# Optimization experiments

Hardware: AMD Instinct MI355X
Metric: run time of the kernel (lower is better)

Reference implementation:

```python
import jax, jax.numpy as jnp
import numpy as np

N = 50000      # nodes
E = 800000     # edges (avg degree 16)
IN = 128       # input feature dim
H = 128        # hidden dim (all layers output H; out_channels unused in source)
DROP_P = 0.5


def setup_inputs() -> dict:
    key = jax.random.key(0)
    ks = jax.random.split(key, 8)
    s_in = 1.0 / np.sqrt(IN).astype(np.float32)
    s_h = 1.0 / np.sqrt(H).astype(np.float32)
    return {
        "x": jax.random.normal(ks[0], (N, IN), jnp.float32),
        "edge_index": jax.random.randint(ks[1], (2, E), 0, N, dtype=jnp.int32),
        "Wl0": jax.random.normal(ks[2], (H, IN), jnp.float32) * s_in,
        "bl0": jnp.zeros((H,), jnp.float32),
        "Wr0": jax.random.normal(ks[3], (H, IN), jnp.float32) * s_in,
        "Wl1": jax.random.normal(ks[4], (H, H), jnp.float32) * s_h,
        "bl1": jnp.zeros((H,), jnp.float32),
        "Wr1": jax.random.normal(ks[5], (H, H), jnp.float32) * s_h,
    }


def _sage_conv(x, src, dst, Wl, bl, Wr):
    # mean-aggregate neighbor messages: gather x[src], scatter-add to dst
    agg = jax.ops.segment_sum(x[src], dst, num_segments=N)          # [N, D]
    deg = jax.ops.segment_sum(jnp.ones((src.shape[0],), x.dtype), dst,
                              num_segments=N)                        # [N]
    agg = agg / jnp.maximum(deg, 1.0)[:, None]                       # scatter_mean (0 for isolated nodes)
    # PyG SAGEConv: lin_l(agg) (with bias) + lin_r(x) (no bias)
    return agg @ Wl.T + bl + x @ Wr.T


def reference(x, edge_index, Wl0, bl0, Wr0, Wl1, bl1, Wr1):
    src, dst = edge_index[0], edge_index[1]
    h = _sage_conv(x, src, dst, Wl0, bl0, Wr0)
    h = jax.nn.relu(h)
    # dropout(p=0.5, training=True) with a fixed key for determinism
    keep = jax.random.bernoulli(jax.random.key(42), 1.0 - DROP_P, h.shape)
    h = jnp.where(keep, h / (1.0 - DROP_P), 0.0)
    out = _sage_conv(h, src, dst, Wl1, bl1, Wr1)
    return out
```

## Files before the change

kernel.cpp:

```cpp
#include <hip/hip_runtime.h>
#include <hip/hip_bf16.h>


#define HDIM 128
#define KDIM 256
#define NBUK 256
#define BNODE 196
#define BCH 2048

typedef __attribute__((ext_vector_type(8))) short bshort8;
typedef __attribute__((ext_vector_type(4))) float f32x4;

__device__ __forceinline__ ushort f2b(float f) {
  __hip_bfloat16 h = __float2bfloat16(f);
  return *(ushort*)&h;
}
__device__ __forceinline__ float blo(unsigned int v) { return __uint_as_float(v << 16); }
__device__ __forceinline__ float bhi(unsigned int v) { return __uint_as_float(v & 0xffff0000u); }
__device__ __forceinline__ unsigned int pack2(float lo, float hi) {
  return (unsigned int)f2b(lo) | ((unsigned int)f2b(hi) << 16);
}

__device__ __forceinline__ unsigned int tf_rotl(unsigned int x, int d) {
  return (x << d) | (x >> (32 - d));
}
__device__ __forceinline__ bool dropout_keep(unsigned int j) {
  unsigned int x0 = 0u, x1 = j;
  const unsigned int ks0 = 0u, ks1 = 42u, ks2 = 0x1BD11BDAu ^ 0u ^ 42u;
  x0 += ks0; x1 += ks1;
#define TF_R(r) { x0 += x1; x1 = tf_rotl(x1, (r)); x1 ^= x0; }
  TF_R(13) TF_R(15) TF_R(26) TF_R(6)
  x0 += ks1; x1 += ks2 + 1u;
  TF_R(17) TF_R(29) TF_R(16) TF_R(24)
  x0 += ks2; x1 += ks0 + 2u;
  TF_R(13) TF_R(15) TF_R(26) TF_R(6)
  x0 += ks0; x1 += ks1 + 3u;
  TF_R(17) TF_R(29) TF_R(16) TF_R(24)
  x0 += ks1; x1 += ks2 + 4u;
  TF_R(13) TF_R(15) TF_R(26) TF_R(6)
  x0 += ks2; x1 += ks0 + 5u;
#undef TF_R
  unsigned int r = x0 ^ x1;
  float u = __uint_as_float((r >> 9) | 0x3f800000u) - 1.0f;
  return u < 0.5f;
}

__global__ __launch_bounds__(256) void bhist_k(const int* __restrict__ dst,
                                               int* __restrict__ bucketCount, int E) {
  __shared__ int h[NBUK];
  h[threadIdx.x] = 0;
  __syncthreads();
  int begin = blockIdx.x * BCH;
  int n = min(BCH, E - begin);
  for (int i = threadIdx.x; i < n; i += 256) atomicAdd(&h[dst[begin + i] / BNODE], 1);
  __syncthreads();
  if (h[threadIdx.x]) atomicAdd(&bucketCount[threadIdx.x], h[threadIdx.x]);
}

__global__ __launch_bounds__(256) void bscan_k(const int* __restrict__ bucketCount,
                                               int* __restrict__ bucketStart,
                                               int* __restrict__ cursor) {
  __shared__ int tmp[NBUK];
  int v = bucketCount[threadIdx.x];
  tmp[threadIdx.x] = v;
  __syncthreads();
  for (int off = 1; off < NBUK; off <<= 1) {
    int t = (threadIdx.x >= off) ? tmp[threadIdx.x - off] : 0;
    __syncthreads();
    tmp[threadIdx.x] += t;
    __syncthreads();
  }
  int ex = tmp[threadIdx.x] - v;
  bucketStart[threadIdx.x] = ex;
  cursor[threadIdx.x] = ex;
}

__global__ __launch_bounds__(256) void bin_k(const int* __restrict__ src,
                                             const int* __restrict__ dst,
                                             int* __restrict__ cursor,
                                             unsigned int* __restrict__ pairs, int E) {
  __shared__ int hist[NBUK];
  __shared__ int lofs[NBUK];
  __shared__ int lcur[NBUK];
  __shared__ int gbase[NBUK];
  __shared__ unsigned int ordv[BCH];
  __shared__ unsigned char ordb[BCH];
  hist[threadIdx.x] = 0;
  __syncthreads();
  int begin = blockIdx.x * BCH;
  int n = min(BCH, E - begin);
  unsigned int vals[BCH / 256];
  int bks[BCH / 256];
  int cnt = 0;
  for (int i = threadIdx.x; i < n; i += 256) {
    int s = src[begin + i], d = dst[begin + i];
    int b = d / BNODE;
    int dloc = d - b * BNODE;
    vals[cnt] = ((unsigned int)s << 8) | (unsigned int)dloc;
    bks[cnt] = b;
    ++cnt;
    atomicAdd(&hist[b], 1);
  }
  __syncthreads();
  {
    int v = hist[threadIdx.x];
    lofs[threadIdx.x] = v;
    __syncthreads();
    for (int off = 1; off < NBUK; off <<= 1) {
      int t = (threadIdx.x >= off) ? lofs[threadIdx.x - off] : 0;
      __syncthreads();
      lofs[threadIdx.x] += t;
      __syncthreads();
    }
    int ex = lofs[threadIdx.x] - v;
    __syncthreads();
    lofs[threadIdx.x] = ex;
    lcur[threadIdx.x] = ex;
    gbase[threadIdx.x] = atomicAdd(&cursor[threadIdx.x], v);
  }
  __syncthreads();
  for (int k = 0; k < cnt; ++k) {
    int b = bks[k];
    int p = atomicAdd(&lcur[b], 1);
    ordv[p] = vals[k];
    ordb[p] = (unsigned char)b;
  }
  __syncthreads();
  for (int j = threadIdx.x; j < n; j += 256) {
    int b = ordb[j];
    pairs[gbase[b] + (j - lofs[b])] = ordv[j];
  }
}

__global__ __launch_bounds__(256) void build_k(const unsigned int* __restrict__ pairs,
                                               const int* __restrict__ bucketStart,
                                               const int* __restrict__ bucketCount,
                                               int* __restrict__ deg,
                                               int* __restrict__ rowptr,
                                               ushort* __restrict__ eidx, int N) {
  __shared__ int h[BNODE];
  __shared__ int lofs[BNODE];
  __shared__ int cur[BNODE];
  const int b = blockIdx.x;
  const int base = bucketStart[b];
  const int cnt = bucketCount[b];
  const int nodebase = b * BNODE;
  const int nloc = min(BNODE, N - nodebase);
  if (threadIdx.x < BNODE) h[threadIdx.x] = 0;
  __syncthreads();
  for (int i = threadIdx.x; i < cnt; i += 256) atomicAdd(&h[pairs[base + i] & 255u], 1);
  __syncthreads();
  if (threadIdx.x < BNODE) lofs[threadIdx.x] = h[threadIdx.x];
  __syncthreads();
  for (int off = 1; off < BNODE; off <<= 1) {
    int t = (threadIdx.x >= off && threadIdx.x < BNODE) ? lofs[threadIdx.x - off] : 0;
    __syncthreads();
    if (threadIdx.x < BNODE) lofs[threadIdx.x] += t;
    __syncthreads();
  }
  if (threadIdx.x < BNODE) {
    int ex = lofs[threadIdx.x] - h[threadIdx.x];
    cur[threadIdx.x] = ex;
    if (threadIdx.x < nloc) {
      deg[nodebase + threadIdx.x] = h[threadIdx.x];
      rowptr[nodebase + threadIdx.x] = base + ex;
    }
  }
  __syncthreads();
  for (int i = threadIdx.x; i < cnt; i += 256) {
    unsigned int v = pairs[base + i];
    int pos = atomicAdd(&cur[v & 255u], 1);
    eidx[base + pos] = (ushort)(v >> 8);
  }
}

__global__ __launch_bounds__(256) void cvt_x_k(const float* __restrict__ x,
                                               ushort* __restrict__ Ab, int N) {
  int t = blockIdx.x * 256 + threadIdx.x;
  if (t >= N * 32) return;
  int n = t >> 5, c4 = t & 31;
  float4 v = *(const float4*)&x[(size_t)n * HDIM + c4 * 4];
  uint2 p;
  p.x = pack2(v.x, v.y);
  p.y = pack2(v.z, v.w);
  *(uint2*)&Ab[(size_t)n * KDIM + HDIM + c4 * 4] = p;
}

__global__ __launch_bounds__(256) void cvt_w_k(const float* __restrict__ Wl0,
                                               const float* __restrict__ Wr0,
                                               const float* __restrict__ Wl1,
                                               const float* __restrict__ Wr1,
                                               ushort* __restrict__ Wc0,
                                               ushort* __restrict__ Wc1) {
  int t = blockIdx.x * 256 + threadIdx.x;
  int o = t >> 7, k = t & 127;
  Wc0[o * KDIM + k] = f2b(Wl0[t]);
  Wc0[o * KDIM + HDIM + k] = f2b(Wr0[t]);
  Wc1[o * KDIM + k] = f2b(Wl1[t]);
  Wc1[o * KDIM + HDIM + k] = f2b(Wr1[t]);
}

__global__ __launch_bounds__(256) void agg_b(const ushort* __restrict__ Xb,
                                             ushort* __restrict__ Ob,
                                             const ushort* __restrict__ eidx,
                                             const int* __restrict__ rowptr,
                                             const int* __restrict__ deg, int N) {
  const int lane = threadIdx.x & 63;
  const int n = blockIdx.x * 4 + (threadIdx.x >> 6);
  if (n >= N) return;
  const int start = rowptr[n];
  const int d = deg[n];
  const int g = lane >> 4;
  const int cl = lane & 15;
  float a0 = 0.f, a1 = 0.f, a2 = 0.f, a3 = 0.f, a4 = 0.f, a5 = 0.f, a6 = 0.f, a7 = 0.f;
  for (int j = 0; j < d; j += 16) {
#pragma unroll
    for (int u = 0; u < 4; ++u) {
      int e = j + u * 4 + g;
      if (e < d) {
        int s = eidx[start + e];
        uint4 v = *(const uint4*)&Xb[(size_t)s * KDIM + HDIM + cl * 8];
        a0 += blo(v.x); a1 += bhi(v.x);
        a2 += blo(v.y); a3 += bhi(v.y);
        a4 += blo(v.z); a5 += bhi(v.z);
        a6 += blo(v.w); a7 += bhi(v.w);
      }
    }
  }
  a0 += __shfl_xor(a0, 16, 64); a0 += __shfl_xor(a0, 32, 64);
  a1 += __shfl_xor(a1, 16, 64); a1 += __shfl_xor(a1, 32, 64);
  a2 += __shfl_xor(a2, 16, 64); a2 += __shfl_xor(a2, 32, 64);
  a3 += __shfl_xor(a3, 16, 64); a3 += __shfl_xor(a3, 32, 64);
  a4 += __shfl_xor(a4, 16, 64); a4 += __shfl_xor(a4, 32, 64);
  a5 += __shfl_xor(a5, 16, 64); a5 += __shfl_xor(a5, 32, 64);
  a6 += __shfl_xor(a6, 16, 64); a6 += __shfl_xor(a6, 32, 64);
  a7 += __shfl_xor(a7, 16, 64); a7 += __shfl_xor(a7, 32, 64);
  if (g == 0) {
    float rd = 1.0f / fmaxf((float)d, 1.0f);
    uint4 p;
    p.x = pack2(a0 * rd, a1 * rd);
    p.y = pack2(a2 * rd, a3 * rd);
    p.z = pack2(a4 * rd, a5 * rd);
    p.w = pack2(a6 * rd, a7 * rd);
    *(uint4*)&Ob[(size_t)n * KDIM + cl * 8] = p;
  }
}

template <int MODE>
__global__ __launch_bounds__(256) void gemm_mfma(const ushort* __restrict__ A,
                                                 const ushort* __restrict__ Wc,
                                                 ushort* __restrict__ hb,
                                                 float* __restrict__ fout,
                                                 const float* __restrict__ bias,
                                                 int N) {
  __shared__ char smem[34816];
  ushort* Wl = (ushort*)smem;
  float* Tl = (float*)smem;
  const int tid = threadIdx.x;
  const int lane = tid & 63;
  const int wid = tid >> 6;
  const int quad = lane >> 4;
  const int l15 = lane & 15;
  const int n0 = blockIdx.x * 64;

  int rowA = n0 + wid * 16 + l15;
  if (rowA >= N) rowA = N - 1;
  bshort8 af[8];
#pragma unroll
  for (int ks = 0; ks < 8; ++ks)
    af[ks] = *(const bshort8*)&A[(size_t)rowA * KDIM + ks * 32 + quad * 8];

  f32x4 acc[8];
#pragma unroll
  for (int i = 0; i < 8; ++i) acc[i] = (f32x4){0.f, 0.f, 0.f, 0.f};

#pragma unroll
  for (int half = 0; half < 2; ++half) {
    __syncthreads();
#pragma unroll
    for (int i = 0; i < 8; ++i) {
      int q = i * 256 + tid;
      int row = q >> 4, seg = q & 15;
      *(uint4*)&Wl[row * 136 + seg * 8] = *(const uint4*)&Wc[row * KDIM + half * HDIM + seg * 8];
    }
    __syncthreads();
#pragma unroll
    for (int ks = 0; ks < 4; ++ks) {
#pragma unroll
      for (int os = 0; os < 8; ++os) {
        bshort8 bf = *(const bshort8*)&Wl[(os * 16 + l15) * 136 + ks * 32 + quad * 8];
        acc[os] = __builtin_amdgcn_mfma_f32_16x16x32_bf16(af[half * 4 + ks], bf, acc[os], 0, 0, 0);
      }
    }
  }

  __syncthreads();

  const int wbase = wid * (16 * 132);
#pragma unroll
  for (int os = 0; os < 8; ++os)
#pragma unroll
    for (int r = 0; r < 4; ++r)
      Tl[wbase + (quad * 4 + r) * 132 + os * 16 + l15] = acc[os][r];

  __syncthreads();

#pragma unroll
  for (int i = 0; i < 8; ++i) {
    int q = i * 64 + lane;
    int r = q >> 5;
    int c4 = q & 31;
    int n = n0 + wid * 16 + r;
    if (n >= N) continue;
    int c = c4 * 4;
    float4 v = *(float4*)&Tl[wbase + r * 132 + c];
    const float4 bv = *(const float4*)&bias[c];
    v.x += bv.x; v.y += bv.y; v.z += bv.z; v.w += bv.w;
    if (MODE == 1) {
      v.x = v.x > 0.0f ? v.x : 0.0f;
      v.y = v.y > 0.0f ? v.y : 0.0f;
      v.z = v.z > 0.0f ? v.z : 0.0f;
      v.w = v.w > 0.0f ? v.w : 0.0f;
      unsigned int fj = (unsigned int)n * HDIM + (unsigned int)c;
      v.x = dropout_keep(fj + 0u) ? v.x * 2.0f : 0.0f;
      v.y = dropout_keep(fj + 1u) ? v.y * 2.0f : 0.0f;
      v.z = dropout_keep(fj + 2u) ? v.z * 2.0f : 0.0f;
      v.w = dropout_keep(fj + 3u) ? v.w * 2.0f : 0.0f;
      uint2 p;
      p.x = pack2(v.x, v.y);
      p.y = pack2(v.z, v.w);
      *(uint2*)&hb[(size_t)n * KDIM + HDIM + c] = p;
    } else {
      *(float4*)&fout[(size_t)n * HDIM + c] = v;
    }
  }
}

extern "C" void kernel_launch(void* const* d_in, const int* in_sizes, int n_in,
                              void* d_out, int out_size, void* d_ws, size_t ws_size,
                              hipStream_t stream) {
  const float* x   = (const float*)d_in[0];
  const int*   ei  = (const int*)d_in[1];
  const float* Wl0 = (const float*)d_in[2];
  const float* bl0 = (const float*)d_in[3];
  const float* Wr0 = (const float*)d_in[4];
  const float* Wl1 = (const float*)d_in[5];
  const float* bl1 = (const float*)d_in[6];
  const float* Wr1 = (const float*)d_in[7];
  float* out = (float*)d_out;

  const int N = in_sizes[0] / HDIM;
  const int E = in_sizes[1] / 2;
  const int* src = ei;
  const int* dst = ei + E;

  const int Na = (N + 63) & ~63;
  int* bucketCount = (int*)d_ws;
  int* bucketStart = bucketCount + NBUK;
  int* cursor      = bucketStart + NBUK;
  int* deg         = cursor + NBUK;
  int* rowptr      = deg + Na;
  unsigned int* pairs = (unsigned int*)(rowptr + Na);
  ushort* eidx     = (ushort*)(pairs + E);
  size_t off = (((size_t)(eidx + E) - (size_t)d_ws) + 255) & ~(size_t)255;
  ushort* Wc0 = (ushort*)((char*)d_ws + off);
  ushort* Wc1 = Wc0 + 128 * KDIM;
  ushort* Ab  = Wc1 + 128 * KDIM;
  ushort* A2  = Ab + (size_t)N * KDIM;

  hipMemsetAsync(bucketCount, 0, NBUK * sizeof(int), stream);

  const int eb = (E + BCH - 1) / BCH;
  const int GB = (N + 63) / 64;
  const int AB = (N + 3) / 4;

  bhist_k<<<eb, 256, 0, stream>>>(dst, bucketCount, E);
  bscan_k<<<1, 256, 0, stream>>>(bucketCount, bucketStart, cursor);
  bin_k<<<eb, 256, 0, stream>>>(src, dst, cursor, pairs, E);
  build_k<<<NBUK, 256, 0, stream>>>(pairs, bucketStart, bucketCount, deg, rowptr, eidx, N);

  cvt_w_k<<<64, 256, 0, stream>>>(Wl0, Wr0, Wl1, Wr1, Wc0, Wc1);
  cvt_x_k<<<(N * 32 + 255) / 256, 256, 0, stream>>>(x, Ab, N);

  agg_b<<<AB, 256, 0, stream>>>(Ab, Ab, eidx, rowptr, deg, N);
  gemm_mfma<1><<<GB, 256, 0, stream>>>(Ab, Wc0, A2, nullptr, bl0, N);
  agg_b<<<AB, 256, 0, stream>>>(A2, A2, eidx, rowptr, deg, N);
  gemm_mfma<2><<<GB, 256, 0, stream>>>(A2, Wc1, nullptr, out, bl1, N);
}
```

Measured before the change: 238.4 us.

## Use fixed-capacity edge buckets and slice aggregation columns across blocks

Drops the separate histogram and scan passes by giving each destination bucket a fixed capacity region, so bin_k atomically reserves slots directly in bucketCount. Rewrites the mean aggregation so each 16-lane group handles one node and a 32-column slice, with four blocks covering the feature dim and 8 edges of gathers in flight per thread. This removes two kernel launches and a pass over dst, and changes the gather pattern to 4-byte loads with more memory-level parallelism. It risks overflow if any bucket exceeds the fixed capacity, and the narrower loads may reduce coalescing efficiency.

```diff
diff --git a/kernel.cpp b/kernel.cpp
--- a/kernel.cpp
+++ b/kernel.cpp
@@ -6,6 +6,7 @@
 #define KDIM 256
 #define NBUK 256
 #define BNODE 196
+#define BCAP 4096
 #define BCH 2048
 
 typedef __attribute__((ext_vector_type(8))) short bshort8;
@@ -45,39 +46,9 @@
   return u < 0.5f;
 }
 
-__global__ __launch_bounds__(256) void bhist_k(const int* __restrict__ dst,
-                                               int* __restrict__ bucketCount, int E) {
-  __shared__ int h[NBUK];
-  h[threadIdx.x] = 0;
-  __syncthreads();
-  int begin = blockIdx.x * BCH;
-  int n = min(BCH, E - begin);
-  for (int i = threadIdx.x; i < n; i += 256) atomicAdd(&h[dst[begin + i] / BNODE], 1);
-  __syncthreads();
-  if (h[threadIdx.x]) atomicAdd(&bucketCount[threadIdx.x], h[threadIdx.x]);
-}
-
-__global__ __launch_bounds__(256) void bscan_k(const int* __restrict__ bucketCount,
-                                               int* __restrict__ bucketStart,
-                                               int* __restrict__ cursor) {
-  __shared__ int tmp[NBUK];
-  int v = bucketCount[threadIdx.x];
-  tmp[threadIdx.x] = v;
-  __syncthreads();
-  for (int off = 1; off < NBUK; off <<= 1) {
-    int t = (threadIdx.x >= off) ? tmp[threadIdx.x - off] : 0;
-    __syncthreads();
-    tmp[threadIdx.x] += t;
-    __syncthreads();
-  }
-  int ex = tmp[threadIdx.x] - v;
-  bucketStart[threadIdx.x] = ex;
-  cursor[threadIdx.x] = ex;
-}
-
 __global__ __launch_bounds__(256) void bin_k(const int* __restrict__ src,
                                              const int* __restrict__ dst,
-                                             int* __restrict__ cursor,
+                                             int* __restrict__ bucketCount,
                                              unsigned int* __restrict__ pairs, int E) {
   __shared__ int hist[NBUK];
   __shared__ int lofs[NBUK];
@@ -116,7 +87,7 @@
     __syncthreads();
     lofs[threadIdx.x] = ex;
     lcur[threadIdx.x] = ex;
-    gbase[threadIdx.x] = atomicAdd(&cursor[threadIdx.x], v);
+    gbase[threadIdx.x] = atomicAdd(&bucketCount[threadIdx.x], v);
   }
   __syncthreads();
   for (int k = 0; k < cnt; ++k) {
@@ -128,12 +99,11 @@
   __syncthreads();
   for (int j = threadIdx.x; j < n; j += 256) {
     int b = ordb[j];
-    pairs[gbase[b] + (j - lofs[b])] = ordv[j];
+    pairs[b * BCAP + gbase[b] + (j - lofs[b])] = ordv[j];
   }
 }
 
 __global__ __launch_bounds__(256) void build_k(const unsigned int* __restrict__ pairs,
-                                               const int* __restrict__ bucketStart,
                                                const int* __restrict__ bucketCount,
                                                int* __restrict__ deg,
                                                int* __restrict__ rowptr,
@@ -142,7 +112,7 @@
   __shared__ int lofs[BNODE];
   __shared__ int cur[BNODE];
   const int b = blockIdx.x;
-  const int base = bucketStart[b];
+  const int base = b * BCAP;
   const int cnt = bucketCount[b];
   const int nodebase = b * BNODE;
   const int nloc = min(BNODE, N - nodebase);
@@ -205,45 +175,34 @@
                                              const ushort* __restrict__ eidx,
                                              const int* __restrict__ rowptr,
                                              const int* __restrict__ deg, int N) {
+  const int slice = blockIdx.x & 3;
+  const int nb = blockIdx.x >> 2;
   const int lane = threadIdx.x & 63;
-  const int n = blockIdx.x * 4 + (threadIdx.x >> 6);
+  const int q = lane >> 4;
+  const int cl = lane & 15;
+  const int n = nb * 16 + (threadIdx.x >> 6) * 4 + q;
   if (n >= N) return;
   const int start = rowptr[n];
   const int d = deg[n];
-  const int g = lane >> 4;
-  const int cl = lane & 15;
-  float a0 = 0.f, a1 = 0.f, a2 = 0.f, a3 = 0.f, a4 = 0.f, a5 = 0.f, a6 = 0.f, a7 = 0.f;
-  for (int j = 0; j < d; j += 16) {
-#pragma unroll
-    for (int u = 0; u < 4; ++u) {
-      int e = j + u * 4 + g;
-      if (e < d) {
-        int s = eidx[start + e];
-        uint4 v = *(const uint4*)&Xb[(size_t)s * KDIM + HDIM + cl * 8];
-        a0 += blo(v.x); a1 += bhi(v.x);
-        a2 += blo(v.y); a3 += bhi(v.y);
-        a4 += blo(v.z); a5 += bhi(v.z);
-        a6 += blo(v.w); a7 += bhi(v.w);
+  const int coff = HDIM + slice * 32 + cl * 2;
+  float a0 = 0.f, a1 = 0.f;
+  for (int j = 0; j < d; j += 8) {
+    unsigned int v[8];
+    bool m[8];
+#pragma unroll
+    for (int u = 0; u < 8; ++u) {
+      m[u] = (j + u) < d;
+      if (m[u]) {
+        int s = eidx[start + j + u];
+        v[u] = *(const unsigned int*)&Xb[(size_t)s * KDIM + coff];
       }
     }
-  }
-  a0 += __shfl_xor(a0, 16, 64); a0 += __shfl_xor(a0, 32, 64);
-  a1 += __shfl_xor(a1, 16, 64); a1 += __shfl_xor(a1, 32, 64);
-  a2 += __shfl_xor(a2, 16, 64); a2 += __shfl_xor(a2, 32, 64);
-  a3 += __shfl_xor(a3, 16, 64); a3 += __shfl_xor(a3, 32, 64);
-  a4 += __shfl_xor(a4, 16, 64); a4 += __shfl_xor(a4, 32, 64);
-  a5 += __shfl_xor(a5, 16, 64); a5 += __shfl_xor(a5, 32, 64);
-  a6 += __shfl_xor(a6, 16, 64); a6 += __shfl_xor(a6, 32, 64);
-  a7 += __shfl_xor(a7, 16, 64); a7 += __shfl_xor(a7, 32, 64);
-  if (g == 0) {
-    float rd = 1.0f / fmaxf((float)d, 1.0f);
-    uint4 p;
-    p.x = pack2(a0 * rd, a1 * rd);
-    p.y = pack2(a2 * rd, a3 * rd);
-    p.z = pack2(a4 * rd, a5 * rd);
-    p.w = pack2(a6 * rd, a7 * rd);
-    *(uint4*)&Ob[(size_t)n * KDIM + cl * 8] = p;
-  }
+#pragma unroll
+    for (int u = 0; u < 8; ++u)
+      if (m[u]) { a0 += blo(v[u]); a1 += bhi(v[u]); }
+  }
+  float rd = 1.0f / fmaxf((float)d, 1.0f);
+  *(unsigned int*)&Ob[(size_t)n * KDIM + slice * 32 + cl * 2] = pack2(a0 * rd, a1 * rd);
 }
 
 template <int MODE>
@@ -356,13 +315,11 @@
 
   const int Na = (N + 63) & ~63;
   int* bucketCount = (int*)d_ws;
-  int* bucketStart = bucketCount + NBUK;
-  int* cursor      = bucketStart + NBUK;
-  int* deg         = cursor + NBUK;
+  int* deg         = bucketCount + NBUK;
   int* rowptr      = deg + Na;
   unsigned int* pairs = (unsigned int*)(rowptr + Na);
-  ushort* eidx     = (ushort*)(pairs + E);
-  size_t off = (((size_t)(eidx + E) - (size_t)d_ws) + 255) & ~(size_t)255;
+  ushort* eidx     = (ushort*)(pairs + NBUK * BCAP);
+  size_t off = (((size_t)(eidx + NBUK * BCAP) - (size_t)d_ws) + 255) & ~(size_t)255;
   ushort* Wc0 = (ushort*)((char*)d_ws + off);
   ushort* Wc1 = Wc0 + 128 * KDIM;
   ushort* Ab  = Wc1 + 128 * KDIM;
@@ -372,12 +329,10 @@
 
   const int eb = (E + BCH - 1) / BCH;
   const int GB = (N + 63) / 64;
-  const int AB = (N + 3) / 4;
-
-  bhist_k<<<eb, 256, 0, stream>>>(dst, bucketCount, E);
-  bscan_k<<<1, 256, 0, stream>>>(bucketCount, bucketStart, cursor);
-  bin_k<<<eb, 256, 0, stream>>>(src, dst, cursor, pairs, E);
-  build_k<<<NBUK, 256, 0, stream>>>(pairs, bucketStart, bucketCount, deg, rowptr, eidx, N);
+  const int AB = 4 * ((N + 15) / 16);
+
+  bin_k<<<eb, 256, 0, stream>>>(src, dst, bucketCount, pairs, E);
+  build_k<<<NBUK, 256, 0, stream>>>(pairs, bucketCount, deg, rowptr, eidx, N);
 
   cvt_w_k<<<64, 256, 0, stream>>>(Wl0, Wr0, Wl1, Wr1, Wc0, Wc1);
   cvt_x_k<<<(N * 32 + 255) / 256, 256, 0, stream>>>(x, Ab, N);
```

Result: slower. 289.3 us (+21.3%).
